# Optimization experiments

Measured on AMD Instinct MI355X. Metric: run time of the kernel, lower is better.

The kernel has to match this reference:

```python
import jax, jax.numpy as jnp
import numpy as np

D, H, L, FF, IN, OUT, S, B = 512, 8, 6, 2048, 32, 3, 512, 32


def setup_inputs() -> dict:
    key = jax.random.key(0)
    ks = iter(jax.random.split(key, 32))
    w = lambda shape: jax.random.normal(next(ks), shape, jnp.float32) * 0.02
    z = lambda shape: jnp.zeros(shape, jnp.float32)
    o = lambda shape: jnp.ones(shape, jnp.float32)
    return {
        'x': jax.random.normal(next(ks), (B, S, IN), jnp.float32),
        'w_in': w((IN, D)), 'b_in': z((D,)), 'g_in': o((D,)), 'be_in': z((D,)),
        'w_qkv': w((L, D, 3 * D)), 'b_qkv': z((L, 3 * D)),
        'w_out': w((L, D, D)), 'b_out': z((L, D)),
        'g1': o((L, D)), 'be1': z((L, D)),
        'w_ff1': w((L, D, FF)), 'b_ff1': z((L, FF)),
        'w_ff2': w((L, FF, D)), 'b_ff2': z((L, D)),
        'g2': o((L, D)), 'be2': z((L, D)),
        'w_h1': w((D, D // 2)), 'b_h1': z((D // 2,)),
        'w_h2': w((D // 2, OUT)), 'b_h2': z((OUT,)),
    }


def _layer_norm(x, g, b, eps=1e-5):
    mu = jnp.mean(x, axis=-1, keepdims=True)
    var = jnp.mean(jnp.square(x - mu), axis=-1, keepdims=True)
    return (x - mu) / jnp.sqrt(var + eps) * g + b


def _gelu(x):
    return jax.nn.gelu(x, approximate=False)  # torch nn.GELU default (erf)


def _pos_encoding(seq_len, d_model):
    pos = jnp.arange(seq_len, dtype=jnp.float32)[:, None]
    div = jnp.exp(jnp.arange(0, d_model, 2, dtype=jnp.float32) * (-np.log(10000.0) / d_model))
    pe = jnp.zeros((seq_len, d_model), jnp.float32)
    pe = pe.at[:, 0::2].set(jnp.sin(pos * div))
    pe = pe.at[:, 1::2].set(jnp.cos(pos * div))
    return pe


def reference(x, w_in, b_in, g_in, be_in, w_qkv, b_qkv, w_out, b_out,
              g1, be1, w_ff1, b_ff1, w_ff2, b_ff2, g2, be2,
              w_h1, b_h1, w_h2, b_h2):
    b, s, _ = x.shape
    d = w_in.shape[1]
    hd = d // H
    scale = hd ** -0.5

    # input projection: Linear -> LayerNorm -> GELU (dropout = identity at eval)
    h = _gelu(_layer_norm(x @ w_in + b_in, g_in, be_in))
    h = h + _pos_encoding(s, d)

    causal_mask = jnp.triu(jnp.ones((s, s), bool), 1)  # True above diagonal = future

    for l in range(w_qkv.shape[0]):
        qkv = (h @ w_qkv[l] + b_qkv[l]).reshape(b, s, 3, H, hd)
        q, k, v = qkv[:, :, 0], qkv[:, :, 1], qkv[:, :, 2]  # [b, s, H, hd]
        scores = jnp.einsum('bihd,bjhd->bhij', q, k) * scale
        scores = jnp.where(causal_mask, -jnp.inf, scores)
        attn = jax.nn.softmax(scores, axis=-1)
        o = jnp.einsum('bhij,bjhd->bihd', attn, v).reshape(b, s, d)
        o = o @ w_out[l] + b_out[l]
        h = _layer_norm(h + o, g1[l], be1[l])
        f = _gelu(h @ w_ff1[l] + b_ff1[l]) @ w_ff2[l] + b_ff2[l]
        h = _layer_norm(h + f, g2[l], be2[l])

    logits = _gelu(h @ w_h1 + b_h1) @ w_h2 + b_h2  # [b, s, OUT]
    return logits[:, -1, :]  # last position only
```

## Files before the change

### kernel.cpp

```cpp
#include <hip/hip_runtime.h>
#include <hip/hip_bf16.h>
#include <math.h>

#define D_   512
#define H_   8
#define HD_  64
#define L_   6
#define FF_  2048
#define IN_  32
#define OUT_ 3
#define S_   512
#define B_   32
#define M_   (B_ * S_)

typedef __attribute__((ext_vector_type(8))) short short8;
typedef __attribute__((ext_vector_type(4))) float floatx4;

__device__ __forceinline__ float gelu_f(float x) {
    const float ax = fabsf(x) * 0.70710678118654752f;
    const float t = __builtin_amdgcn_rcpf(fmaf(0.3275911f, ax, 1.0f));
    float p = fmaf(1.061405429f, t, -1.453152027f);
    p = fmaf(p, t, 1.421413741f);
    p = fmaf(p, t, -0.284496736f);
    p = fmaf(p, t, 0.254829592f);
    p = p * t;
    const float e = __expf(-ax * ax);
    const float er = copysignf(fmaf(-p, e, 1.0f), x);
    return 0.5f * x * (1.0f + er);
}
__device__ __forceinline__ float bf2f(unsigned short u) {
    union { unsigned int i; float f; } c; c.i = ((unsigned)u) << 16; return c.f;
}
__device__ __forceinline__ unsigned short f2bf(float v) {
    __hip_bfloat16 t = __float2bfloat16(v);
    return *(unsigned short*)&t;
}
__device__ __forceinline__ void async16(const void* g, void* l) {
    __builtin_amdgcn_global_load_lds(
        (const __attribute__((address_space(1))) unsigned int*)g,
        (__attribute__((address_space(3))) unsigned int*)l, 16, 0, 0);
}
__device__ __forceinline__ void stage2(const short* g, char* d, long rs) {
    async16(g, d);
    async16(g + rs, d + 8192);
}

#define MFMA_ROW(ai, accr)                                                    \
    accr[0] = __builtin_amdgcn_mfma_f32_16x16x32_bf16(ai, b[0], accr[0], 0, 0, 0); \
    accr[1] = __builtin_amdgcn_mfma_f32_16x16x32_bf16(ai, b[1], accr[1], 0, 0, 0); \
    accr[2] = __builtin_amdgcn_mfma_f32_16x16x32_bf16(ai, b[2], accr[2], 0, 0, 0); \
    accr[3] = __builtin_amdgcn_mfma_f32_16x16x32_bf16(ai, b[3], accr[3], 0, 0, 0);

#define MFMA_PHASE(B0)                                                        \
    __builtin_amdgcn_s_barrier();                                             \
    asm volatile("s_waitcnt lgkmcnt(0)" ::: "memory");                        \
    __builtin_amdgcn_sched_barrier(0);                                        \
    __builtin_amdgcn_s_setprio(1);                                            \
    MFMA_ROW(a[0], acc[B0 + 0])                                               \
    MFMA_ROW(a[1], acc[B0 + 1])                                               \
    MFMA_ROW(a[2], acc[B0 + 2])                                               \
    MFMA_ROW(a[3], acc[B0 + 3])                                               \
    __builtin_amdgcn_s_setprio(0);

template<int DO_GELU, int OUT_BF16, int ADD_RES>
__global__ __launch_bounds__(512, 2)
void gemm_mfma256_k(const __hip_bfloat16* __restrict__ A,
                    const __hip_bfloat16* __restrict__ WT,
                    const float* __restrict__ bias,
                    const float* __restrict__ R,
                    void* __restrict__ C,
                    int N, int K) {
    __shared__ __align__(16) char smem[131072];

    const int tid  = threadIdx.x;
    const int lane = tid & 63;
    const int wave = tid >> 6;

    const int Lid = blockIdx.y * gridDim.x + blockIdx.x;
    const int xcd = Lid & 7;
    const int idx = Lid >> 3;
    const int gx  = gridDim.x, gy8 = gridDim.y >> 3;
    const int m0 = (xcd * gy8 + idx / gx) * 256;
    const int n0 = (idx % gx) * 256;

    const int wm = (wave >> 2) * 128;
    const int wn = (wave & 3) * 64;
    const int r = lane & 15, q = lane >> 4;
    const int qa = (q ^ (r & 3)) * 8;

    const int srow = tid >> 2;
    const int sc = ((tid & 3) ^ (srow & 3)) * 8;
    const short* Ag = (const short*)A + (long)(m0 + srow) * K + sc;
    const short* Bg = (const short*)WT + (long)(n0 + srow) * K + sc;
    const long rs = (long)128 * K;

    floatx4 acc[8][4];
    #pragma unroll
    for (int i = 0; i < 8; i++)
        #pragma unroll
        for (int j = 0; j < 4; j++) acc[i][j] = (floatx4)0.f;

    const int NT = K >> 6;

    stage2(Ag,      smem         + tid * 16, rs);
    stage2(Bg,      smem + 32768 + tid * 16, rs);
    stage2(Ag + 32, smem + 16384 + tid * 16, rs);
    stage2(Bg + 32, smem + 49152 + tid * 16, rs);
    asm volatile("s_waitcnt vmcnt(4)" ::: "memory");
    __builtin_amdgcn_s_barrier();

    short8 a[4], b[4];
    for (int t = 0; t < NT; ++t) {
        const int cur = t & 1, nxt = cur ^ 1;
        const bool hn = (t + 1 < NT);
        const short* As = (const short*)(smem + cur * 65536);
        const short* Bs = (const short*)(smem + cur * 65536 + 32768);
        const short* Agt = Ag + (t + 1) * 64;
        const short* Bgt = Bg + (t + 1) * 64;
        char* Ad = smem + nxt * 65536;
        char* Bd = smem + nxt * 65536 + 32768;

        #pragma unroll
        for (int i = 0; i < 4; i++)
            a[i] = *(const short8*)&As[(wm + i * 16 + r) * 32 + qa];
        #pragma unroll
        for (int j = 0; j < 4; j++)
            b[j] = *(const short8*)&Bs[(wn + j * 16 + r) * 32 + qa];
        if (hn) stage2(Agt, Ad + tid * 16, rs);
        MFMA_PHASE(0)
        __builtin_amdgcn_s_barrier();

        #pragma unroll
        for (int i = 0; i < 4; i++)
            a[i] = *(const short8*)&As[(wm + 64 + i * 16 + r) * 32 + qa];
        if (hn) stage2(Bgt, Bd + tid * 16, rs);
        MFMA_PHASE(4)
        if (hn) asm volatile("s_waitcnt vmcnt(4)" ::: "memory");
        else    asm volatile("s_waitcnt vmcnt(0)" ::: "memory");
        __builtin_amdgcn_s_barrier();

        #pragma unroll
        for (int i = 0; i < 4; i++)
            a[i] = *(const short8*)&As[8192 + (wm + i * 16 + r) * 32 + qa];
        #pragma unroll
        for (int j = 0; j < 4; j++)
            b[j] = *(const short8*)&Bs[8192 + (wn + j * 16 + r) * 32 + qa];
        if (hn) stage2(Agt + 32, Ad + 16384 + tid * 16, rs);
        MFMA_PHASE(0)
        __builtin_amdgcn_s_barrier();

        #pragma unroll
        for (int i = 0; i < 4; i++)
            a[i] = *(const short8*)&As[8192 + (wm + 64 + i * 16 + r) * 32 + qa];
        if (hn) stage2(Bgt + 32, Bd + 16384 + tid * 16, rs);
        MFMA_PHASE(4)
        if (hn) asm volatile("s_waitcnt vmcnt(4)" ::: "memory");
        __builtin_amdgcn_s_barrier();
    }

    float* Ef = (float*)smem;
    const int erow = tid >> 3;
    const int ej = tid & 7;
    #pragma unroll
    for (int ch = 0; ch < 4; ch++) {
        __builtin_amdgcn_s_barrier();
        if ((wave >> 2) == (ch >> 1)) {
            #pragma unroll
            for (int mf2 = 0; mf2 < 4; mf2++) {
                const int mf = (ch & 1) * 4 + mf2;
                #pragma unroll
                for (int nf = 0; nf < 4; nf++)
                    #pragma unroll
                    for (int rg = 0; rg < 4; rg++)
                        Ef[(mf2 * 16 + q * 4 + rg) * 260 + wn + nf * 16 + r] =
                            acc[mf][nf][rg];
            }
        }
        __builtin_amdgcn_s_barrier();
        #pragma unroll
        for (int e = 0; e < 8; e++) {
            const int c4 = ej + e * 8;
            const long grow = (long)(m0 + ch * 64 + erow) * N + n0 + c4 * 4;
            const float4 v = *(const float4*)&Ef[erow * 260 + c4 * 4];
            const float4 bv = *(const float4*)&bias[n0 + c4 * 4];
            float o0 = v.x + bv.x, o1 = v.y + bv.y;
            float o2 = v.z + bv.z, o3 = v.w + bv.w;
            if (DO_GELU) {
                o0 = gelu_f(o0); o1 = gelu_f(o1);
                o2 = gelu_f(o2); o3 = gelu_f(o3);
            }
            if (ADD_RES) {
                const float4 rv = *(const float4*)&R[grow];
                o0 += rv.x; o1 += rv.y; o2 += rv.z; o3 += rv.w;
            }
            if (OUT_BF16) {
                ushort4 pk;
                pk.x = f2bf(o0); pk.y = f2bf(o1);
                pk.z = f2bf(o2); pk.w = f2bf(o3);
                *(ushort4*)((unsigned short*)C + grow) = pk;
            } else {
                *(float4*)((float*)C + grow) = make_float4(o0, o1, o2, o3);
            }
        }
    }
}

template<int DO_GELU, int OUT_BF16, int ADD_RES, int PIPE>
__global__ __launch_bounds__(256)
void gemm_mfma_k(const __hip_bfloat16* __restrict__ A,
                 const __hip_bfloat16* __restrict__ WT,
                 const float* __restrict__ bias,
                 const float* __restrict__ R,
                 void* __restrict__ C,
                 int N, int K) {
    __shared__ __align__(16) char smem[PIPE ? 65536 : 34816];
    float* Ep = (float*)smem;

    const int tid  = threadIdx.x;
    const int lane = tid & 63;
    const int wave = tid >> 6;

    const int Lid = blockIdx.y * gridDim.x + blockIdx.x;
    const int xcd = Lid & 7;
    const int idx = Lid >> 3;
    const int gx  = gridDim.x, gy8 = gridDim.y >> 3;
    const int m0 = (xcd * gy8 + idx / gx) * 128;
    const int n0 = (idx % gx) * 128;

    const int wm = (wave >> 1) * 64, wn = (wave & 1) * 64;

    const int srow = tid >> 2;
    const int scol = ((tid & 3) ^ (srow & 3)) * 8;
    const short* Ag = (const short*)A + (long)(m0 + srow) * K + scol;
    const short* Bg = (const short*)WT + (long)(n0 + srow) * K + scol;

    floatx4 acc[4][4];
    #pragma unroll
    for (int i = 0; i < 4; i++)
        #pragma unroll
        for (int j = 0; j < 4; j++) acc[i][j] = (floatx4)0.f;

    const int r = lane & 15, q = lane >> 4;
    const int qa = (q ^ (r & 3)) * 8;

    if (PIPE) {
        const int nIter = K >> 6;
        {
            short* As_ = (short*)smem;
            short* Bs_ = (short*)(smem + 16384);
            async16(Ag,                     As_ + tid * 8);
            async16(Ag + (long)64 * K,      As_ + 2048 + tid * 8);
            async16(Ag + 32,                As_ + 4096 + tid * 8);
            async16(Ag + (long)64 * K + 32, As_ + 6144 + tid * 8);
            async16(Bg,                     Bs_ + tid * 8);
            async16(Bg + (long)64 * K,      Bs_ + 2048 + tid * 8);
            async16(Bg + 32,                Bs_ + 4096 + tid * 8);
            async16(Bg + (long)64 * K + 32, Bs_ + 6144 + tid * 8);
        }
        for (int i = 0; i < nIter; i++) {
            __syncthreads();
            if (i + 1 < nIter) {
                const int k0 = (i + 1) << 6;
                short* As_ = (short*)(smem + ((i + 1) & 1) * 32768);
                short* Bs_ = (short*)(smem + ((i + 1) & 1) * 32768 + 16384);
                async16(Ag + k0,                     As_ + tid * 8);
                async16(Ag + (long)64 * K + k0,      As_ + 2048 + tid * 8);
                async16(Ag + k0 + 32,                As_ + 4096 + tid * 8);
                async16(Ag + (long)64 * K + k0 + 32, As_ + 6144 + tid * 8);
                async16(Bg + k0,                     Bs_ + tid * 8);
                async16(Bg + (long)64 * K + k0,      Bs_ + 2048 + tid * 8);
                async16(Bg + k0 + 32,                Bs_ + 4096 + tid * 8);
                async16(Bg + (long)64 * K + k0 + 32, Bs_ + 6144 + tid * 8);
            }
            const short* As_ = (const short*)(smem + (i & 1) * 32768);
            const short* Bs_ = (const short*)(smem + (i & 1) * 32768 + 16384);
            #pragma unroll
            for (int c = 0; c < 2; c++) {
                const short* Asc = As_ + c * 4096;
                const short* Bsc = Bs_ + c * 4096;
                short8 af[4], bf[4];
                #pragma unroll
                for (int t = 0; t < 4; t++)
                    af[t] = *(const short8*)&Asc[(wm + t * 16 + r) * 32 + qa];
                #pragma unroll
                for (int t = 0; t < 4; t++)
                    bf[t] = *(const short8*)&Bsc[(wn + t * 16 + r) * 32 + qa];
                #pragma unroll
                for (int i2 = 0; i2 < 4; i2++)
                    #pragma unroll
                    for (int j = 0; j < 4; j++)
                        acc[i2][j] = __builtin_amdgcn_mfma_f32_16x16x32_bf16(
                            af[i2], bf[j], acc[i2][j], 0, 0, 0);
            }
        }
        __syncthreads();
    } else {
        short* As0 = (short*)(smem);
        short* As1 = (short*)(smem + 8192);
        short* Bs0 = (short*)(smem + 16384);
        short* Bs1 = (short*)(smem + 24576);
        for (int k0 = 0; k0 < K; k0 += 64) {
            async16(Ag + k0,                     As0 + tid * 8);
            async16(Ag + (long)64 * K + k0,      As0 + 2048 + tid * 8);
            async16(Ag + k0 + 32,                As1 + tid * 8);
            async16(Ag + (long)64 * K + k0 + 32, As1 + 2048 + tid * 8);
            async16(Bg + k0,                     Bs0 + tid * 8);
            async16(Bg + (long)64 * K + k0,      Bs0 + 2048 + tid * 8);
            async16(Bg + k0 + 32,                Bs1 + tid * 8);
            async16(Bg + (long)64 * K + k0 + 32, Bs1 + 2048 + tid * 8);
            __syncthreads();
            #pragma unroll
            for (int c = 0; c < 2; c++) {
                const short* Asc = c ? As1 : As0;
                const short* Bsc = c ? Bs1 : Bs0;
                short8 af[4], bf[4];
                #pragma unroll
                for (int t = 0; t < 4; t++)
                    af[t] = *(const short8*)&Asc[(wm + t * 16 + r) * 32 + qa];
                #pragma unroll
                for (int t = 0; t < 4; t++)
                    bf[t] = *(const short8*)&Bsc[(wn + t * 16 + r) * 32 + qa];
                #pragma unroll
                for (int i = 0; i < 4; i++)
                    #pragma unroll
                    for (int j = 0; j < 4; j++)
                        acc[i][j] = __builtin_amdgcn_mfma_f32_16x16x32_bf16(
                            af[i], bf[j], acc[i][j], 0, 0, 0);
            }
            __syncthreads();
        }
    }

    const int erow = tid >> 5;
    const int ecol = (tid & 31) * 4;
    const float4 bvec = *(const float4*)&bias[n0 + ecol];

    #pragma unroll
    for (int pass = 0; pass < 2; pass++) {
        if (pass) __syncthreads();
        if ((wave >> 1) == pass) {
            #pragma unroll
            for (int i = 0; i < 4; i++)
                #pragma unroll
                for (int j = 0; j < 4; j++)
                    #pragma unroll
                    for (int rg = 0; rg < 4; rg++)
                        Ep[(i * 16 + q * 4 + rg) * 132 + wn + j * 16 + r] =
                            acc[i][j][rg];
        }
        __syncthreads();
        #pragma unroll
        for (int it = 0; it < 8; it++) {
            const int row = it * 8 + erow;
            const long grow = (long)(m0 + pass * 64 + row) * N + n0 + ecol;
            const float4 v = *(const float4*)&Ep[row * 132 + ecol];
            float o0 = v.x + bvec.x, o1 = v.y + bvec.y;
            float o2 = v.z + bvec.z, o3 = v.w + bvec.w;
            if (DO_GELU) {
                o0 = gelu_f(o0); o1 = gelu_f(o1);
                o2 = gelu_f(o2); o3 = gelu_f(o3);
            }
            if (ADD_RES) {
                const float4 rv = *(const float4*)&R[grow];
                o0 += rv.x; o1 += rv.y; o2 += rv.z; o3 += rv.w;
            }
            if (OUT_BF16) {
                ushort4 pk;
                pk.x = f2bf(o0); pk.y = f2bf(o1);
                pk.z = f2bf(o2); pk.w = f2bf(o3);
                *(ushort4*)((unsigned short*)C + grow) = pk;
            } else {
                *(float4*)((float*)C + grow) = make_float4(o0, o1, o2, o3);
            }
        }
    }
}

__global__ __launch_bounds__(256)
void transpose_cast_k(const float* __restrict__ W, __hip_bfloat16* __restrict__ WT,
                      int K, int N) {
    __shared__ float tile[32][33];
    const float* Wl = W + (long)blockIdx.z * K * N;
    __hip_bfloat16* WTl = WT + (long)blockIdx.z * K * N;
    const int n0 = blockIdx.x * 32, k0 = blockIdx.y * 32;
    const int tx = threadIdx.x & 31, ty = threadIdx.x >> 5;
    for (int rr = ty; rr < 32; rr += 8)
        tile[rr][tx] = Wl[(long)(k0 + rr) * N + n0 + tx];
    __syncthreads();
    for (int rr = ty; rr < 32; rr += 8)
        WTl[(long)(n0 + rr) * K + k0 + tx] = __float2bfloat16(tile[tx][rr]);
}

template<int DO_GELU>
__global__ __launch_bounds__(256)
void gemm_bias_k(const float* __restrict__ A, long lda,
                 const float* __restrict__ W,
                 const float* __restrict__ bias,
                 float* __restrict__ C,
                 int M, int N, int K) {
    __shared__ float As[16][64];
    __shared__ float Ws[16][64];
    const int tx = threadIdx.x;
    const int ty = threadIdx.y;
    const int tid = ty * 16 + tx;
    const int m0 = blockIdx.y * 64;
    const int n0 = blockIdx.x * 64;
    float acc[4][4] = {};
    for (int k0 = 0; k0 < K; k0 += 16) {
        #pragma unroll
        for (int e = tid; e < 64 * 16; e += 256) {
            int m = e >> 4, k = e & 15;
            float v = 0.f;
            if (m0 + m < M) v = A[(long)(m0 + m) * lda + k0 + k];
            As[k][m] = v;
        }
        #pragma unroll
        for (int e = tid; e < 16 * 64; e += 256) {
            int k = e >> 6, n = e & 63;
            float v = 0.f;
            if (n0 + n < N) v = W[(long)(k0 + k) * N + n0 + n];
            Ws[k][n] = v;
        }
        __syncthreads();
        #pragma unroll
        for (int kk = 0; kk < 16; kk++) {
            float a[4], w[4];
            #pragma unroll
            for (int i = 0; i < 4; i++) a[i] = As[kk][ty * 4 + i];
            #pragma unroll
            for (int j = 0; j < 4; j++) w[j] = Ws[kk][tx * 4 + j];
            #pragma unroll
            for (int i = 0; i < 4; i++)
                #pragma unroll
                for (int j = 0; j < 4; j++)
                    acc[i][j] += a[i] * w[j];
        }
        __syncthreads();
    }
    #pragma unroll
    for (int i = 0; i < 4; i++) {
        int m = m0 + ty * 4 + i;
        if (m >= M) continue;
        #pragma unroll
        for (int j = 0; j < 4; j++) {
            int n = n0 + tx * 4 + j;
            if (n >= N) continue;
            float v = acc[i][j] + bias[n];
            if (DO_GELU) v = gelu_f(v);
            C[(long)m * N + n] = v;
        }
    }
}

__global__ __launch_bounds__(256)
void ln_k(const float* __restrict__ X,
          const float* __restrict__ g,
          const float* __restrict__ be,
          float* __restrict__ H,
          __hip_bfloat16* __restrict__ Hb) {
    const int row = blockIdx.x * 4 + (threadIdx.x >> 6);
    const int lane = threadIdx.x & 63;
    const float* xp = X + (long)row * D_ + lane * 8;
    const float4 a = *(const float4*)xp;
    const float4 c = *(const float4*)(xp + 4);
    float s = a.x + a.y + a.z + a.w + c.x + c.y + c.z + c.w;
    #pragma unroll
    for (int off = 1; off < 64; off <<= 1) s += __shfl_xor(s, off);
    const float mu = s * (1.0f / D_);
    float d[8] = { a.x - mu, a.y - mu, a.z - mu, a.w - mu,
                   c.x - mu, c.y - mu, c.z - mu, c.w - mu };
    float ss = 0.f;
    #pragma unroll
    for (int e = 0; e < 8; e++) ss += d[e] * d[e];
    #pragma unroll
    for (int off = 1; off < 64; off <<= 1) ss += __shfl_xor(ss, off);
    const float inv = 1.0f / sqrtf(ss * (1.0f / D_) + 1e-5f);
    const float4 g0 = *(const float4*)(g + lane * 8);
    const float4 g1 = *(const float4*)(g + lane * 8 + 4);
    const float4 e0 = *(const float4*)(be + lane * 8);
    const float4 e1 = *(const float4*)(be + lane * 8 + 4);
    const float gv[8] = { g0.x, g0.y, g0.z, g0.w, g1.x, g1.y, g1.z, g1.w };
    const float ev[8] = { e0.x, e0.y, e0.z, e0.w, e1.x, e1.y, e1.z, e1.w };
    float o[8];
    short8 pk;
    #pragma unroll
    for (int e = 0; e < 8; e++) {
        o[e] = d[e] * inv * gv[e] + ev[e];
        pk[e] = (short)f2bf(o[e]);
    }
    float* hp = H + (long)row * D_ + lane * 8;
    *(float4*)hp = make_float4(o[0], o[1], o[2], o[3]);
    *(float4*)(hp + 4) = make_float4(o[4], o[5], o[6], o[7]);
    *(short8*)((unsigned short*)Hb + (long)row * D_ + lane * 8) = pk;
}

__global__ __launch_bounds__(256)
void ln_gelu_pos_k(const float* __restrict__ X,
                   const float* __restrict__ g,
                   const float* __restrict__ be,
                   float* __restrict__ Hout,
                   __hip_bfloat16* __restrict__ Hb) {
    const int row = blockIdx.x;
    const int s = row & (S_ - 1);
    const int t = threadIdx.x;
    const float* x = X + (long)row * D_;
    float v0 = x[t], v1 = x[t + 256];
    __shared__ float red[256];
    red[t] = v0 + v1;
    __syncthreads();
    for (int off = 128; off; off >>= 1) {
        if (t < off) red[t] += red[t + off];
        __syncthreads();
    }
    float mu = red[0] * (1.0f / D_);
    __syncthreads();
    float d0 = v0 - mu, d1 = v1 - mu;
    red[t] = d0 * d0 + d1 * d1;
    __syncthreads();
    for (int off = 128; off; off >>= 1) {
        if (t < off) red[t] += red[t + off];
        __syncthreads();
    }
    float var = red[0] * (1.0f / D_);
    float inv = 1.0f / sqrtf(var + 1e-5f);
    float o0 = gelu_f(d0 * inv * g[t] + be[t]);
    float o1 = gelu_f(d1 * inv * g[t + 256] + be[t + 256]);
    {
        int d = t, i = d >> 1;
        float dv = expf((float)(2 * i) * (-9.210340371976184f / 512.0f));
        float ang = (float)s * dv;
        o0 += (d & 1) ? cosf(ang) : sinf(ang);
    }
    {
        int d = t + 256, i = d >> 1;
        float dv = expf((float)(2 * i) * (-9.210340371976184f / 512.0f));
        float ang = (float)s * dv;
        o1 += (d & 1) ? cosf(ang) : sinf(ang);
    }
    Hout[(long)row * D_ + t] = o0;
    Hout[(long)row * D_ + t + 256] = o1;
    Hb[(long)row * D_ + t] = __float2bfloat16(o0);
    Hb[(long)row * D_ + t + 256] = __float2bfloat16(o1);
}

#define LDT 72
__global__ __launch_bounds__(256)
void attn_mfma_k(const __hip_bfloat16* __restrict__ qkv,
                 __hip_bfloat16* __restrict__ O) {
    const int qt = blockIdx.x;
    const int bh = blockIdx.y;
    const int b = bh >> 3, h = bh & (H_ - 1);
    const int tid = threadIdx.x;
    const int wave = tid >> 6, lane = tid & 63;
    const int ln = lane & 15, quad = lane >> 4;
    const int wm = wave * 32;
    const int i0 = qt * 128;

    __shared__ unsigned short Qs[128 * LDT];
    __shared__ unsigned short Ks[64 * LDT];
    __shared__ unsigned short Vt[64 * LDT];
    __shared__ unsigned short Ps[128 * LDT];
    __shared__ float stat[128];

    const unsigned short* base = (const unsigned short*)qkv + (long)b * S_ * (3 * D_);

    {
        const int r0 = tid >> 3, c0 = (tid & 7) * 8;
        #pragma unroll
        for (int i = 0; i < 4; i++) {
            const int rw = i * 32 + r0;
            *(short8*)&Qs[rw * LDT + c0] =
                *(const short8*)(base + (long)(i0 + rw) * (3 * D_) + h * HD_ + c0);
        }
    }

    float m_i[2] = { -INFINITY, -INFINITY };
    float l_i[2] = { 0.f, 0.f };
    floatx4 o_acc[2][4];
    #pragma unroll
    for (int i = 0; i < 2; i++)
        #pragma unroll
        for (int j = 0; j < 4; j++) o_acc[i][j] = (floatx4)0.f;

    const int kr = tid >> 2, kc = (tid & 3) * 16;
    const int vj = tid & 63, vc = (tid >> 6) * 16;

    const int ktmax = 2 * qt + 1;
    for (int kt = 0; kt <= ktmax; kt++) {
        const int j0 = kt * 64;
        {
            const unsigned short* kp = base + (long)(j0 + kr) * (3 * D_) + D_ + h * HD_ + kc;
            *(short8*)&Ks[kr * LDT + kc]     = *(const short8*)(kp);
            *(short8*)&Ks[kr * LDT + kc + 8] = *(const short8*)(kp + 8);
            const unsigned short* vp = base + (long)(j0 + vj) * (3 * D_) + 2 * D_ + h * HD_ + vc;
            short8 v0 = *(const short8*)(vp);
            short8 v1 = *(const short8*)(vp + 8);
            #pragma unroll
            for (int e = 0; e < 8; e++) {
                Vt[(vc + e) * LDT + vj]     = (unsigned short)v0[e];
                Vt[(vc + 8 + e) * LDT + vj] = (unsigned short)v1[e];
            }
        }
        __syncthreads();

        floatx4 sa[4][2];
        #pragma unroll
        for (int mt = 0; mt < 4; mt++)
            #pragma unroll
            for (int nt = 0; nt < 2; nt++) sa[mt][nt] = (floatx4)0.f;
        #pragma unroll
        for (int c = 0; c < 2; c++) {
            short8 kf[4], qf[2];
            #pragma unroll
            for (int mt = 0; mt < 4; mt++)
                kf[mt] = *(const short8*)&Ks[(mt * 16 + ln) * LDT + c * 32 + quad * 8];
            #pragma unroll
            for (int nt = 0; nt < 2; nt++)
                qf[nt] = *(const short8*)&Qs[(wm + nt * 16 + ln) * LDT + c * 32 + quad * 8];
            #pragma unroll
            for (int mt = 0; mt < 4; mt++)
                #pragma unroll
                for (int nt = 0; nt < 2; nt++)
                    sa[mt][nt] = __builtin_amdgcn_mfma_f32_16x16x32_bf16(
                        kf[mt], qf[nt], sa[mt][nt], 0, 0, 0);
        }

        const bool domask = (kt >= 2 * qt);
        #pragma unroll
        for (int nt = 0; nt < 2; nt++) {
            const int qg = i0 + wm + nt * 16 + ln;
            float mx = -INFINITY;
            #pragma unroll
            for (int mt = 0; mt < 4; mt++)
                #pragma unroll
                for (int rg = 0; rg < 4; rg++) {
                    float v = sa[mt][nt][rg] * 0.125f;
                    if (domask && (j0 + mt * 16 + quad * 4 + rg > qg)) v = -INFINITY;
                    sa[mt][nt][rg] = v;
                    mx = fmaxf(mx, v);
                }
            mx = fmaxf(mx, __shfl_xor(mx, 16));
            mx = fmaxf(mx, __shfl_xor(mx, 32));
            const float mn = fmaxf(m_i[nt], mx);
            const float alpha = __expf(m_i[nt] - mn);
            m_i[nt] = mn;
            float ls = 0.f;
            #pragma unroll
            for (int mt = 0; mt < 4; mt++) {
                ushort4 pk;
                float p0 = __expf(sa[mt][nt][0] - mn);
                float p1 = __expf(sa[mt][nt][1] - mn);
                float p2 = __expf(sa[mt][nt][2] - mn);
                float p3 = __expf(sa[mt][nt][3] - mn);
                ls += p0 + p1 + p2 + p3;
                pk.x = f2bf(p0); pk.y = f2bf(p1); pk.z = f2bf(p2); pk.w = f2bf(p3);
                *(ushort4*)&Ps[(wm + nt * 16 + ln) * LDT + mt * 16 + quad * 4] = pk;
            }
            ls += __shfl_xor(ls, 16);
            ls += __shfl_xor(ls, 32);
            l_i[nt] = l_i[nt] * alpha + ls;
            if (quad == 0) stat[wm + nt * 16 + ln] = alpha;
        }

        #pragma unroll
        for (int mt2 = 0; mt2 < 2; mt2++) {
            #pragma unroll
            for (int rg = 0; rg < 4; rg++) {
                const float a = stat[wm + mt2 * 16 + quad * 4 + rg];
                #pragma unroll
                for (int nt = 0; nt < 4; nt++) o_acc[mt2][nt][rg] *= a;
            }
        }

        #pragma unroll
        for (int c = 0; c < 2; c++) {
            short8 pf[2], vf[4];
            #pragma unroll
            for (int mt2 = 0; mt2 < 2; mt2++)
                pf[mt2] = *(const short8*)&Ps[(wm + mt2 * 16 + ln) * LDT + c * 32 + quad * 8];
            #pragma unroll
            for (int nt = 0; nt < 4; nt++)
                vf[nt] = *(const short8*)&Vt[(nt * 16 + ln) * LDT + c * 32 + quad * 8];
            #pragma unroll
            for (int mt2 = 0; mt2 < 2; mt2++)
                #pragma unroll
                for (int nt = 0; nt < 4; nt++)
                    o_acc[mt2][nt] = __builtin_amdgcn_mfma_f32_16x16x32_bf16(
                        pf[mt2], vf[nt], o_acc[mt2][nt], 0, 0, 0);
        }
        __syncthreads();
    }

    if (quad == 0) {
        stat[wm + ln]      = l_i[0];
        stat[wm + 16 + ln] = l_i[1];
    }
    unsigned short* Og = (unsigned short*)O;
    #pragma unroll
    for (int mt2 = 0; mt2 < 2; mt2++) {
        #pragma unroll
        for (int rg = 0; rg < 4; rg++) {
            const float linv = 1.0f / stat[wm + mt2 * 16 + quad * 4 + rg];
            const long row = (long)(b * S_ + i0 + wm + mt2 * 16 + quad * 4 + rg);
            #pragma unroll
            for (int nt = 0; nt < 4; nt++)
                Og[row * D_ + h * HD_ + nt * 16 + ln] =
                    f2bf(o_acc[mt2][nt][rg] * linv);
        }
    }
}

__global__ __launch_bounds__(256)
void head1_k(const float* __restrict__ h, const float* __restrict__ w1,
             const float* __restrict__ b1, float* __restrict__ th) {
    __shared__ float hs[D_];
    const int b = blockIdx.x, n = threadIdx.x;
    const float* hr = h + (long)(b * S_ + S_ - 1) * D_;
    hs[n] = hr[n];
    hs[n + 256] = hr[n + 256];
    __syncthreads();
    float s = 0.f;
    #pragma unroll 8
    for (int k = 0; k < D_; k++) s += hs[k] * w1[(long)k * 256 + n];
    th[b * 256 + n] = gelu_f(s + b1[n]);
}

__global__ __launch_bounds__(64)
void head2_k(const float* __restrict__ th, const float* __restrict__ w2,
             const float* __restrict__ b2, float* __restrict__ out) {
    const int b = blockIdx.x, lane = threadIdx.x;
    const float* t = th + b * 256;
    float s0 = 0.f, s1 = 0.f, s2 = 0.f;
    #pragma unroll
    for (int e = 0; e < 4; e++) {
        const int k = lane * 4 + e;
        const float tv = t[k];
        s0 += tv * w2[k * 3 + 0];
        s1 += tv * w2[k * 3 + 1];
        s2 += tv * w2[k * 3 + 2];
    }
    #pragma unroll
    for (int off = 1; off < 64; off <<= 1) {
        s0 += __shfl_xor(s0, off);
        s1 += __shfl_xor(s1, off);
        s2 += __shfl_xor(s2, off);
    }
    if (lane == 0) {
        out[b * 3 + 0] = s0 + b2[0];
        out[b * 3 + 1] = s1 + b2[1];
        out[b * 3 + 2] = s2 + b2[2];
    }
}

extern "C" void kernel_launch(void* const* d_in, const int* in_sizes, int n_in,
                              void* d_out, int out_size, void* d_ws, size_t ws_size,
                              hipStream_t stream) {
    const float* x     = (const float*)d_in[0];
    const float* w_in  = (const float*)d_in[1];
    const float* b_in  = (const float*)d_in[2];
    const float* g_in  = (const float*)d_in[3];
    const float* be_in = (const float*)d_in[4];
    const float* w_qkv = (const float*)d_in[5];
    const float* b_qkv = (const float*)d_in[6];
    const float* w_out = (const float*)d_in[7];
    const float* b_out = (const float*)d_in[8];
    const float* g1    = (const float*)d_in[9];
    const float* be1   = (const float*)d_in[10];
    const float* w_ff1 = (const float*)d_in[11];
    const float* b_ff1 = (const float*)d_in[12];
    const float* w_ff2 = (const float*)d_in[13];
    const float* b_ff2 = (const float*)d_in[14];
    const float* g2    = (const float*)d_in[15];
    const float* be2   = (const float*)d_in[16];
    const float* w_h1  = (const float*)d_in[17];
    const float* b_h1  = (const float*)d_in[18];
    const float* w_h2  = (const float*)d_in[19];
    const float* b_h2  = (const float*)d_in[20];
    float* out = (float*)d_out;

    float* h    = (float*)d_ws;
    float* bufB = h + (long)M_ * D_;
    float* th   = bufB + (long)M_ * D_;
    __hip_bfloat16* hb    = (__hip_bfloat16*)(th + 32 * 256);
    __hip_bfloat16* attb  = hb + (long)M_ * D_;
    __hip_bfloat16* bufAb = attb + (long)M_ * D_;
    __hip_bfloat16* qkvT  = bufAb + (long)M_ * FF_;
    __hip_bfloat16* outT  = qkvT + (long)L_ * (3 * D_) * D_;
    __hip_bfloat16* ff1T  = outT + (long)L_ * D_ * D_;
    __hip_bfloat16* ff2T  = ff1T + (long)L_ * FF_ * D_;

    dim3 blk(16, 16);

    transpose_cast_k<<<dim3((3 * D_) / 32, D_ / 32, L_), 256, 0, stream>>>(w_qkv, qkvT, D_, 3 * D_);
    transpose_cast_k<<<dim3(D_ / 32, D_ / 32, L_), 256, 0, stream>>>(w_out, outT, D_, D_);
    transpose_cast_k<<<dim3(FF_ / 32, D_ / 32, L_), 256, 0, stream>>>(w_ff1, ff1T, D_, FF_);
    transpose_cast_k<<<dim3(D_ / 32, FF_ / 32, L_), 256, 0, stream>>>(w_ff2, ff2T, FF_, D_);

    gemm_bias_k<0><<<dim3(D_ / 64, M_ / 64), blk, 0, stream>>>(
        x, IN_, w_in, b_in, bufB, M_, D_, IN_);
    ln_gelu_pos_k<<<M_, 256, 0, stream>>>(bufB, g_in, be_in, h, hb);

    for (int l = 0; l < L_; l++) {
        gemm_mfma256_k<0, 1, 0><<<dim3((3 * D_) / 256, M_ / 256), 512, 0, stream>>>(
            hb, qkvT + (long)l * (3 * D_) * D_, b_qkv + l * 3 * D_, nullptr,
            bufAb, 3 * D_, D_);
        attn_mfma_k<<<dim3(S_ / 128, B_ * H_), 256, 0, stream>>>(bufAb, attb);
        gemm_mfma_k<0, 0, 1, 1><<<dim3(D_ / 128, M_ / 128), 256, 0, stream>>>(
            attb, outT + (long)l * D_ * D_, b_out + l * D_, h,
            bufB, D_, D_);
        ln_k<<<M_ / 4, 256, 0, stream>>>(bufB, g1 + l * D_, be1 + l * D_, h, hb);
        gemm_mfma256_k<1, 1, 0><<<dim3(FF_ / 256, M_ / 256), 512, 0, stream>>>(
            hb, ff1T + (long)l * FF_ * D_, b_ff1 + l * FF_, nullptr,
            bufAb, FF_, D_);
        gemm_mfma_k<0, 0, 1, 1><<<dim3(D_ / 128, M_ / 128), 256, 0, stream>>>(
            bufAb, ff2T + (long)l * D_ * FF_, b_ff2 + l * D_, h,
            bufB, D_, FF_);
        ln_k<<<M_ / 4, 256, 0, stream>>>(bufB, g2 + l * D_, be2 + l * D_, h, hb);
    }

    head1_k<<<B_, 256, 0, stream>>>(h, w_h1, b_h1, th);
    head2_k<<<B_, 64, 0, stream>>>(th, w_h2, b_h2, out);
}
```

Baseline: 1.669 ms.

## Rewrite 128-tile GEMM with split-K async double-buffer pipeline and new LDS swizzle

The 128x128 GEMM kernel now uses a two-half K pipeline: it prefetches the next tile half into a double buffer with async global-to-LDS loads, and uses vmcnt waits instead of full syncthreads. Both GEMM kernels switch to an LDS swizzle keyed on (r>>1)&3 to cut bank conflicts. The explicit lgkmcnt wait and sched barrier are removed from the 256-tile MFMA phase. The QKV projection moves from the 256-tile kernel to the 128-tile kernel for more blocks, and launch bounds now request 2 blocks per CU. Dropping the lgkmcnt wait relies on the compiler inserting the correct waits for the LDS reads.

New measurement: 1.661 ms. About the same (-0.5%).

```diff
diff --git a/kernel.cpp b/kernel.cpp
--- a/kernel.cpp
+++ b/kernel.cpp
@@ -40,10 +40,11 @@
         (const __attribute__((address_space(1))) unsigned int*)g,
         (__attribute__((address_space(3))) unsigned int*)l, 16, 0, 0);
 }
-__device__ __forceinline__ void stage2(const short* g, char* d, long rs) {
+__device__ __forceinline__ void stage2(const short* g, char* d, long rs, int off2) {
     async16(g, d);
-    async16(g + rs, d + 8192);
-}
+    async16(g + rs, d + off2);
+}
+
 
 #define MFMA_ROW(ai, accr)                                                    \
     accr[0] = __builtin_amdgcn_mfma_f32_16x16x32_bf16(ai, b[0], accr[0], 0, 0, 0); \
@@ -53,8 +54,6 @@
 
 #define MFMA_PHASE(B0)                                                        \
     __builtin_amdgcn_s_barrier();                                             \
-    asm volatile("s_waitcnt lgkmcnt(0)" ::: "memory");                        \
-    __builtin_amdgcn_sched_barrier(0);                                        \
     __builtin_amdgcn_s_setprio(1);                                            \
     MFMA_ROW(a[0], acc[B0 + 0])                                               \
     MFMA_ROW(a[1], acc[B0 + 1])                                               \
@@ -86,10 +85,10 @@
     const int wm = (wave >> 2) * 128;
     const int wn = (wave & 3) * 64;
     const int r = lane & 15, q = lane >> 4;
-    const int qa = (q ^ (r & 3)) * 8;
+    const int qa = (q ^ ((r >> 1) & 3)) * 8;
 
     const int srow = tid >> 2;
-    const int sc = ((tid & 3) ^ (srow & 3)) * 8;
+    const int sc = ((tid & 3) ^ ((tid >> 3) & 3)) * 8;
     const short* Ag = (const short*)A + (long)(m0 + srow) * K + sc;
     const short* Bg = (const short*)WT + (long)(n0 + srow) * K + sc;
     const long rs = (long)128 * K;
@@ -102,10 +101,10 @@
 
     const int NT = K >> 6;
 
-    stage2(Ag,      smem         + tid * 16, rs);
-    stage2(Bg,      smem + 32768 + tid * 16, rs);
-    stage2(Ag + 32, smem + 16384 + tid * 16, rs);
-    stage2(Bg + 32, smem + 49152 + tid * 16, rs);
+    stage2(Ag,      smem         + tid * 16, rs, 8192);
+    stage2(Bg,      smem + 32768 + tid * 16, rs, 8192);
+    stage2(Ag + 32, smem + 16384 + tid * 16, rs, 8192);
+    stage2(Bg + 32, smem + 49152 + tid * 16, rs, 8192);
     asm volatile("s_waitcnt vmcnt(4)" ::: "memory");
     __builtin_amdgcn_s_barrier();
 
@@ -126,14 +125,14 @@
         #pragma unroll
         for (int j = 0; j < 4; j++)
             b[j] = *(const short8*)&Bs[(wn + j * 16 + r) * 32 + qa];
-        if (hn) stage2(Agt, Ad + tid * 16, rs);
+        if (hn) stage2(Agt, Ad + tid * 16, rs, 8192);
         MFMA_PHASE(0)
         __builtin_amdgcn_s_barrier();
 
         #pragma unroll
         for (int i = 0; i < 4; i++)
             a[i] = *(const short8*)&As[(wm + 64 + i * 16 + r) * 32 + qa];
-        if (hn) stage2(Bgt, Bd + tid * 16, rs);
+        if (hn) stage2(Bgt, Bd + tid * 16, rs, 8192);
         MFMA_PHASE(4)
         if (hn) asm volatile("s_waitcnt vmcnt(4)" ::: "memory");
         else    asm volatile("s_waitcnt vmcnt(0)" ::: "memory");
@@ -145,14 +144,14 @@
         #pragma unroll
         for (int j = 0; j < 4; j++)
             b[j] = *(const short8*)&Bs[8192 + (wn + j * 16 + r) * 32 + qa];
-        if (hn) stage2(Agt + 32, Ad + 16384 + tid * 16, rs);
+        if (hn) stage2(Agt + 32, Ad + 16384 + tid * 16, rs, 8192);
         MFMA_PHASE(0)
         __builtin_amdgcn_s_barrier();
 
         #pragma unroll
         for (int i = 0; i < 4; i++)
             a[i] = *(const short8*)&As[8192 + (wm + 64 + i * 16 + r) * 32 + qa];
-        if (hn) stage2(Bgt + 32, Bd + 16384 + tid * 16, rs);
+        if (hn) stage2(Bgt + 32, Bd + 16384 + tid * 16, rs, 8192);
         MFMA_PHASE(4)
         if (hn) asm volatile("s_waitcnt vmcnt(4)" ::: "memory");
         __builtin_amdgcn_s_barrier();
@@ -205,15 +204,15 @@
     }
 }
 
-template<int DO_GELU, int OUT_BF16, int ADD_RES, int PIPE>
-__global__ __launch_bounds__(256)
+template<int DO_GELU, int OUT_BF16, int ADD_RES>
+__global__ __launch_bounds__(256, 2)
 void gemm_mfma_k(const __hip_bfloat16* __restrict__ A,
                  const __hip_bfloat16* __restrict__ WT,
                  const float* __restrict__ bias,
                  const float* __restrict__ R,
                  void* __restrict__ C,
                  int N, int K) {
-    __shared__ __align__(16) char smem[PIPE ? 65536 : 34816];
+    __shared__ __align__(16) char smem[65536];
     float* Ep = (float*)smem;
 
     const int tid  = threadIdx.x;
@@ -228,11 +227,14 @@
     const int n0 = (idx % gx) * 128;
 
     const int wm = (wave >> 1) * 64, wn = (wave & 1) * 64;
+    const int r = lane & 15, q = lane >> 4;
+    const int qa = (q ^ ((r >> 1) & 3)) * 8;
 
     const int srow = tid >> 2;
-    const int scol = ((tid & 3) ^ (srow & 3)) * 8;
-    const short* Ag = (const short*)A + (long)(m0 + srow) * K + scol;
-    const short* Bg = (const short*)WT + (long)(n0 + srow) * K + scol;
+    const int sc = ((tid & 3) ^ ((tid >> 3) & 3)) * 8;
+    const short* Ag = (const short*)A + (long)(m0 + srow) * K + sc;
+    const short* Bg = (const short*)WT + (long)(n0 + srow) * K + sc;
+    const long rs = (long)64 * K;
 
     floatx4 acc[4][4];
     #pragma unroll
@@ -240,95 +242,69 @@
         #pragma unroll
         for (int j = 0; j < 4; j++) acc[i][j] = (floatx4)0.f;
 
-    const int r = lane & 15, q = lane >> 4;
-    const int qa = (q ^ (r & 3)) * 8;
-
-    if (PIPE) {
-        const int nIter = K >> 6;
-        {
-            short* As_ = (short*)smem;
-            short* Bs_ = (short*)(smem + 16384);
-            async16(Ag,                     As_ + tid * 8);
-            async16(Ag + (long)64 * K,      As_ + 2048 + tid * 8);
-            async16(Ag + 32,                As_ + 4096 + tid * 8);
-            async16(Ag + (long)64 * K + 32, As_ + 6144 + tid * 8);
-            async16(Bg,                     Bs_ + tid * 8);
-            async16(Bg + (long)64 * K,      Bs_ + 2048 + tid * 8);
-            async16(Bg + 32,                Bs_ + 4096 + tid * 8);
-            async16(Bg + (long)64 * K + 32, Bs_ + 6144 + tid * 8);
-        }
-        for (int i = 0; i < nIter; i++) {
-            __syncthreads();
-            if (i + 1 < nIter) {
-                const int k0 = (i + 1) << 6;
-                short* As_ = (short*)(smem + ((i + 1) & 1) * 32768);
-                short* Bs_ = (short*)(smem + ((i + 1) & 1) * 32768 + 16384);
-                async16(Ag + k0,                     As_ + tid * 8);
-                async16(Ag + (long)64 * K + k0,      As_ + 2048 + tid * 8);
-                async16(Ag + k0 + 32,                As_ + 4096 + tid * 8);
-                async16(Ag + (long)64 * K + k0 + 32, As_ + 6144 + tid * 8);
-                async16(Bg + k0,                     Bs_ + tid * 8);
-                async16(Bg + (long)64 * K + k0,      Bs_ + 2048 + tid * 8);
-                async16(Bg + k0 + 32,                Bs_ + 4096 + tid * 8);
-                async16(Bg + (long)64 * K + k0 + 32, Bs_ + 6144 + tid * 8);
-            }
-            const short* As_ = (const short*)(smem + (i & 1) * 32768);
-            const short* Bs_ = (const short*)(smem + (i & 1) * 32768 + 16384);
-            #pragma unroll
-            for (int c = 0; c < 2; c++) {
-                const short* Asc = As_ + c * 4096;
-                const short* Bsc = Bs_ + c * 4096;
-                short8 af[4], bf[4];
-                #pragma unroll
-                for (int t = 0; t < 4; t++)
-                    af[t] = *(const short8*)&Asc[(wm + t * 16 + r) * 32 + qa];
-                #pragma unroll
-                for (int t = 0; t < 4; t++)
-                    bf[t] = *(const short8*)&Bsc[(wn + t * 16 + r) * 32 + qa];
-                #pragma unroll
-                for (int i2 = 0; i2 < 4; i2++)
-                    #pragma unroll
-                    for (int j = 0; j < 4; j++)
-                        acc[i2][j] = __builtin_amdgcn_mfma_f32_16x16x32_bf16(
-                            af[i2], bf[j], acc[i2][j], 0, 0, 0);
-            }
-        }
-        __syncthreads();
-    } else {
-        short* As0 = (short*)(smem);
-        short* As1 = (short*)(smem + 8192);
-        short* Bs0 = (short*)(smem + 16384);
-        short* Bs1 = (short*)(smem + 24576);
-        for (int k0 = 0; k0 < K; k0 += 64) {
-            async16(Ag + k0,                     As0 + tid * 8);
-            async16(Ag + (long)64 * K + k0,      As0 + 2048 + tid * 8);
-            async16(Ag + k0 + 32,                As1 + tid * 8);
-            async16(Ag + (long)64 * K + k0 + 32, As1 + 2048 + tid * 8);
-            async16(Bg + k0,                     Bs0 + tid * 8);
-            async16(Bg + (long)64 * K + k0,      Bs0 + 2048 + tid * 8);
-            async16(Bg + k0 + 32,                Bs1 + tid * 8);
-            async16(Bg + (long)64 * K + k0 + 32, Bs1 + 2048 + tid * 8);
-            __syncthreads();
-            #pragma unroll
-            for (int c = 0; c < 2; c++) {
-                const short* Asc = c ? As1 : As0;
-                const short* Bsc = c ? Bs1 : Bs0;
-                short8 af[4], bf[4];
-                #pragma unroll
-                for (int t = 0; t < 4; t++)
-                    af[t] = *(const short8*)&Asc[(wm + t * 16 + r) * 32 + qa];
-                #pragma unroll
-                for (int t = 0; t < 4; t++)
-                    bf[t] = *(const short8*)&Bsc[(wn + t * 16 + r) * 32 + qa];
-                #pragma unroll
-                for (int i = 0; i < 4; i++)
-                    #pragma unroll
-                    for (int j = 0; j < 4; j++)
-                        acc[i][j] = __builtin_amdgcn_mfma_f32_16x16x32_bf16(
-                            af[i], bf[j], acc[i][j], 0, 0, 0);
-            }
-            __syncthreads();
-        }
+    const int NT = K >> 6;
+
+    stage2(Ag,      smem + 0     + tid * 16, rs, 4096);
+    stage2(Bg,      smem + 16384 + tid * 16, rs, 4096);
+    stage2(Ag + 32, smem + 8192  + tid * 16, rs, 4096);
+    stage2(Bg + 32, smem + 24576 + tid * 16, rs, 4096);
+    asm volatile("s_waitcnt vmcnt(4)" ::: "memory");
+    __builtin_amdgcn_s_barrier();
+    __builtin_amdgcn_sched_barrier(0);
+
+    short8 a[4], b[4];
+    for (int t = 0; t < NT; ++t) {
+        const int cur = t & 1, nxt = cur ^ 1;
+        const bool hn = (t + 1 < NT);
+        const short* As = (const short*)(smem + cur * 32768);
+        const short* Bs = (const short*)(smem + cur * 32768 + 16384);
+        const short* Agt = Ag + (t + 1) * 64;
+        const short* Bgt = Bg + (t + 1) * 64;
+        char* Ad = smem + nxt * 32768;
+        char* Bd = smem + nxt * 32768 + 16384;
+
+        if (hn) {
+            stage2(Agt, Ad + tid * 16, rs, 4096);
+            stage2(Bgt, Bd + tid * 16, rs, 4096);
+        }
+        #pragma unroll
+        for (int i = 0; i < 4; i++)
+            a[i] = *(const short8*)&As[(wm + i * 16 + r) * 32 + qa];
+        #pragma unroll
+        for (int j = 0; j < 4; j++)
+            b[j] = *(const short8*)&Bs[(wn + j * 16 + r) * 32 + qa];
+        #pragma unroll
+        for (int i = 0; i < 4; i++)
+            #pragma unroll
+            for (int j = 0; j < 4; j++)
+                acc[i][j] = __builtin_amdgcn_mfma_f32_16x16x32_bf16(
+                    a[i], b[j], acc[i][j], 0, 0, 0);
+        __builtin_amdgcn_sched_barrier(0);
+        if (hn) asm volatile("s_waitcnt vmcnt(4)" ::: "memory");
+        else    asm volatile("s_waitcnt vmcnt(0)" ::: "memory");
+        __builtin_amdgcn_s_barrier();
+        __builtin_amdgcn_sched_barrier(0);
+
+        if (hn) {
+            stage2(Agt + 32, Ad + 8192 + tid * 16, rs, 4096);
+            stage2(Bgt + 32, Bd + 8192 + tid * 16, rs, 4096);
+        }
+        #pragma unroll
+        for (int i = 0; i < 4; i++)
+            a[i] = *(const short8*)&As[4096 + (wm + i * 16 + r) * 32 + qa];
+        #pragma unroll
+        for (int j = 0; j < 4; j++)
+            b[j] = *(const short8*)&Bs[4096 + (wn + j * 16 + r) * 32 + qa];
+        #pragma unroll
+        for (int i = 0; i < 4; i++)
+            #pragma unroll
+            for (int j = 0; j < 4; j++)
+                acc[i][j] = __builtin_amdgcn_mfma_f32_16x16x32_bf16(
+                    a[i], b[j], acc[i][j], 0, 0, 0);
+        __builtin_amdgcn_sched_barrier(0);
+        if (hn) asm volatile("s_waitcnt vmcnt(4)" ::: "memory");
+        __builtin_amdgcn_s_barrier();
+        __builtin_amdgcn_sched_barrier(0);
     }
 
     const int erow = tid >> 5;
@@ -801,18 +777,18 @@
     ln_gelu_pos_k<<<M_, 256, 0, stream>>>(bufB, g_in, be_in, h, hb);
 
     for (int l = 0; l < L_; l++) {
-        gemm_mfma256_k<0, 1, 0><<<dim3((3 * D_) / 256, M_ / 256), 512, 0, stream>>>(
+        gemm_mfma_k<0, 1, 0><<<dim3((3 * D_) / 128, M_ / 128), 256, 0, stream>>>(
             hb, qkvT + (long)l * (3 * D_) * D_, b_qkv + l * 3 * D_, nullptr,
             bufAb, 3 * D_, D_);
         attn_mfma_k<<<dim3(S_ / 128, B_ * H_), 256, 0, stream>>>(bufAb, attb);
-        gemm_mfma_k<0, 0, 1, 1><<<dim3(D_ / 128, M_ / 128), 256, 0, stream>>>(
+        gemm_mfma_k<0, 0, 1><<<dim3(D_ / 128, M_ / 128), 256, 0, stream>>>(
             attb, outT + (long)l * D_ * D_, b_out + l * D_, h,
             bufB, D_, D_);
         ln_k<<<M_ / 4, 256, 0, stream>>>(bufB, g1 + l * D_, be1 + l * D_, h, hb);
         gemm_mfma256_k<1, 1, 0><<<dim3(FF_ / 256, M_ / 256), 512, 0, stream>>>(
             hb, ff1T + (long)l * FF_ * D_, b_ff1 + l * FF_, nullptr,
             bufAb, FF_, D_);
-        gemm_mfma_k<0, 0, 1, 1><<<dim3(D_ / 128, M_ / 128), 256, 0, stream>>>(
+        gemm_mfma_k<0, 0, 1><<<dim3(D_ / 128, M_ / 128), 256, 0, stream>>>(
             bufAb, ff2T + (long)l * D_ * FF_, b_ff2 + l * D_, h,
             bufB, D_, FF_);
         ln_k<<<M_ / 4, 256, 0, stream>>>(bufB, g2 + l * D_, be2 + l * D_, h, hb);
```
